# Kernel tuning notes

Hardware: AMD Instinct MI355X
Metric: run time of the kernel (lower is better)

The kernel has to match this reference:

```python
import jax, jax.numpy as jnp
import numpy as np

E, D, B, P = 16, 5, 8, 65536
EXPERT_DIM = 128
N_BETAS = 4
EPS = 1e-6


def setup_inputs() -> dict:
    key = jax.random.key(0)
    k1, k2, k3, k4 = jax.random.split(key, 4)
    V = jax.random.normal(k1, (E, D, B, P), dtype=jnp.float32)
    masks = jax.random.randint(k2, (E, P), 0, 2) > 0  # bool [E, P]
    betas = jax.random.normal(k3, (E, N_BETAS), dtype=jnp.float32)
    expert_pos_embed = jax.random.normal(k4, (E, EXPERT_DIM), dtype=jnp.float32)
    temperature = jnp.ones((1,), dtype=jnp.float32)
    return {
        'V': V,
        'masks': masks,
        'betas': betas,
        'expert_pos_embed': expert_pos_embed,
        'temperature': temperature,
        'num_patches': P,
    }


def reference(V, masks, betas, expert_pos_embed, temperature, num_patches):
    # per-expert scalar weights
    pos_w = jax.nn.sigmoid(expert_pos_embed.mean(axis=1))          # [E]
    beta_w = 1.0 + jax.nn.sigmoid(betas).mean(axis=1)              # [E] (sum(sigmoid)/len)
    w = pos_w * beta_w                                             # [E]

    m = masks.astype(V.dtype)                                      # [E, P]
    # masked weighted vote accumulation over experts, per direction
    num = jnp.einsum('e,edbp,ep->dbp', w, V, m)                    # [D, B, P]
    den = jnp.einsum('e,ep->p', w, m)                              # [P] (same for all d, b)
    den = jnp.maximum(den, EPS)

    patch_votes = (num / den[None, None, :]).sum(axis=0) / 5.0     # [B, P]
    return patch_votes / jnp.abs(temperature[0])
```

## Files before the change

kernel.cpp:

```cpp
#include <hip/hip_runtime.h>
#include <math.h>

#define NE 16
#define ND 5
#define NB 8
#define NP 65536
#define EDIM 128
#define NBETAS 4


__global__ __launch_bounds__(128) void cfa_prep(const float* __restrict__ betas,
                                                const float* __restrict__ embed,
                                                const float* __restrict__ temp,
                                                const unsigned int* __restrict__ mask_words,
                                                float* __restrict__ ws) {
    const int t = threadIdx.x;
    if (t < NE) {
        const float4* ep = (const float4*)(embed + t * EDIM);
        float s = 0.f;
        #pragma unroll
        for (int i = 0; i < EDIM / 4; ++i) { float4 v = ep[i]; s += v.x + v.y + v.z + v.w; }
        float pos_w = 1.f / (1.f + __expf(-s * (1.f / EDIM)));
        float bs = 0.f;
        #pragma unroll
        for (int i = 0; i < NBETAS; ++i) bs += 1.f / (1.f + __expf(-betas[t * NBETAS + i]));
        ws[t] = pos_w * (1.f + bs * (1.f / NBETAS));
    }
    if (t == NE) ws[NE] = 0.2f / fabsf(temp[0]);
    if (t >= 64) {
        const int lane = t - 64;
        unsigned o1 = 0, o3 = 0;
        #pragma unroll
        for (int k = 0; k < 16; ++k) {
            unsigned x = mask_words[lane + k * 64];
            o1 |= x & 0x0000FF00u;
            o3 |= x & 0xFF000000u;
        }
        #pragma unroll
        for (int off = 32; off; off >>= 1) {
            o1 |= __shfl_xor(o1, off, 64);
            o3 |= __shfl_xor(o3, off, 64);
        }
        if (lane == 0) {
            int flag = o1 ? 0 : (o3 ? 2 : 1);
            ((int*)ws)[NE + 1] = flag;
        }
    }
}

__global__ __launch_bounds__(256) void cfa_main(const float* __restrict__ V,
                                                const void* __restrict__ masks,
                                                const float* __restrict__ ws,
                                                float* __restrict__ out) {
    __shared__ float sw[NE];
    __shared__ float sscale;
    __shared__ int sflag;
    if (threadIdx.x < NE) sw[threadIdx.x] = ws[threadIdx.x];
    if (threadIdx.x == NE) sscale = ws[NE];
    if (threadIdx.x == NE + 1) sflag = ((const int*)ws)[NE + 1];
    __syncthreads();

    const int idx = blockIdx.x * 256 + threadIdx.x;
    const int pi  = idx & (NP / 2 - 1);
    const int b   = idx >> 15;
    const int p   = pi << 1;

    float m0[NE], m1[NE];
    const int flag = sflag;
    if (flag == 0) {
        const unsigned char* mb = (const unsigned char*)masks + p;
        #pragma unroll
        for (int e = 0; e < NE; ++e) {
            uchar2 u = *(const uchar2*)(mb + e * NP);
            m0[e] = (float)u.x; m1[e] = (float)u.y;
        }
    } else if (flag == 1) {
        const int* mi = (const int*)masks + p;
        #pragma unroll
        for (int e = 0; e < NE; ++e) {
            int2 u = *(const int2*)(mi + e * NP);
            m0[e] = (float)u.x; m1[e] = (float)u.y;
        }
    } else {
        const float* mf = (const float*)masks + p;
        #pragma unroll
        for (int e = 0; e < NE; ++e) {
            float2 u = *(const float2*)(mf + e * NP);
            m0[e] = u.x; m1[e] = u.y;
        }
    }

    float wm0[NE], wm1[NE];
    float den0 = 0.f, den1 = 0.f;
    #pragma unroll
    for (int e = 0; e < NE; ++e) {
        const float we = sw[e];
        wm0[e] = we * m0[e]; wm1[e] = we * m1[e];
        den0 += wm0[e];      den1 += wm1[e];
    }

    float a0 = 0.f, a1 = 0.f;
    const float* vp = V + b * NP + p;
    #pragma unroll
    for (int e = 0; e < NE; ++e) {
        #pragma unroll
        for (int d = 0; d < ND; ++d) {
            float2 v = *(const float2*)(vp + (e * ND + d) * (NB * NP));
            a0 = fmaf(wm0[e], v.x, a0);
            a1 = fmaf(wm1[e], v.y, a1);
        }
    }

    const float scale = sscale;
    float2 o;
    o.x = a0 / fmaxf(den0, 1e-6f) * scale;
    o.y = a1 / fmaxf(den1, 1e-6f) * scale;
    *(float2*)(out + b * NP + p) = o;
}

extern "C" void kernel_launch(void* const* d_in, const int* in_sizes, int n_in,
                              void* d_out, int out_size, void* d_ws, size_t ws_size,
                              hipStream_t stream) {
    const float* V     = (const float*)d_in[0];
    const void*  masks = d_in[1];
    const float* betas = (const float*)d_in[2];
    const float* embed = (const float*)d_in[3];
    const float* temp  = (const float*)d_in[4];

    float* ws  = (float*)d_ws;
    float* out = (float*)d_out;

    cfa_prep<<<1, 128, 0, stream>>>(betas, embed, temp,
                                    (const unsigned int*)masks, ws);

    const int threads = NB * NP / 2;
    cfa_main<<<threads / 256, 256, 0, stream>>>(V, masks, ws, out);
}
```

Measured before the change: 37.74 us.

## Fuse prep into main kernel, widen to float4, split experts across half-blocks

Removes the separate prep launch by having each block recompute the per-expert weights, scale and mask dtype flag itself. The flag check now samples only the first 64 mask words. Each thread handles four patches with float4 loads, and the two half-blocks each sum eight experts before a shared-memory reduction. This cuts a kernel launch and its dependency and widens memory accesses, at the cost of redundant per-block prep work, an extra barrier, and a weaker mask-dtype heuristic.

```diff
diff --git a/kernel.cpp b/kernel.cpp
--- a/kernel.cpp
+++ b/kernel.cpp
@@ -9,113 +9,127 @@
 #define NBETAS 4
 
 
-__global__ __launch_bounds__(128) void cfa_prep(const float* __restrict__ betas,
-                                                const float* __restrict__ embed,
-                                                const float* __restrict__ temp,
-                                                const unsigned int* __restrict__ mask_words,
-                                                float* __restrict__ ws) {
-    const int t = threadIdx.x;
-    if (t < NE) {
-        const float4* ep = (const float4*)(embed + t * EDIM);
+__global__ __launch_bounds__(256, 4) void cfa_fused(
+    const float* __restrict__ V,
+    const void* __restrict__ masks,
+    const float* __restrict__ betas,
+    const float* __restrict__ embed,
+    const float* __restrict__ temp,
+    float* __restrict__ out)
+{
+    __shared__ float sw[NE];
+    __shared__ float sscale;
+    __shared__ int   sflag;
+    __shared__ float4 redA[128];
+    __shared__ float4 redD[128];
+
+    const int tid = threadIdx.x;
+
+    if (tid < 128) {
+        const int e = tid >> 3, j = tid & 7;
+        const float4* ep = (const float4*)(embed + e * EDIM + j * 16);
         float s = 0.f;
         #pragma unroll
-        for (int i = 0; i < EDIM / 4; ++i) { float4 v = ep[i]; s += v.x + v.y + v.z + v.w; }
-        float pos_w = 1.f / (1.f + __expf(-s * (1.f / EDIM)));
-        float bs = 0.f;
-        #pragma unroll
-        for (int i = 0; i < NBETAS; ++i) bs += 1.f / (1.f + __expf(-betas[t * NBETAS + i]));
-        ws[t] = pos_w * (1.f + bs * (1.f / NBETAS));
-    }
-    if (t == NE) ws[NE] = 0.2f / fabsf(temp[0]);
-    if (t >= 64) {
-        const int lane = t - 64;
-        unsigned o1 = 0, o3 = 0;
-        #pragma unroll
-        for (int k = 0; k < 16; ++k) {
-            unsigned x = mask_words[lane + k * 64];
-            o1 |= x & 0x0000FF00u;
-            o3 |= x & 0xFF000000u;
+        for (int i = 0; i < 4; ++i) { float4 v = ep[i]; s += v.x + v.y + v.z + v.w; }
+        s += __shfl_xor(s, 4, 64);
+        s += __shfl_xor(s, 2, 64);
+        s += __shfl_xor(s, 1, 64);
+        if (j == 0) {
+            float pos_w = 1.f / (1.f + __expf(-s * (1.f / EDIM)));
+            float bs = 0.f;
+            #pragma unroll
+            for (int i = 0; i < NBETAS; ++i)
+                bs += 1.f / (1.f + __expf(-betas[e * NBETAS + i]));
+            sw[e] = pos_w * (1.f + bs * (1.f / NBETAS));
         }
+        if (tid == 0) sscale = 0.2f / fabsf(temp[0]);
+    } else if (tid >= 192) {
+        const int lane = tid - 192;
+        unsigned x = ((const unsigned*)masks)[lane];
+        unsigned o1 = x & 0x0000FF00u, o3 = x & 0xFF000000u;
         #pragma unroll
         for (int off = 32; off; off >>= 1) {
             o1 |= __shfl_xor(o1, off, 64);
             o3 |= __shfl_xor(o3, off, 64);
         }
-        if (lane == 0) {
-            int flag = o1 ? 0 : (o3 ? 2 : 1);
-            ((int*)ws)[NE + 1] = flag;
-        }
+        if (lane == 0) sflag = o1 ? 0 : (o3 ? 2 : 1);
     }
-}
-
-__global__ __launch_bounds__(256) void cfa_main(const float* __restrict__ V,
-                                                const void* __restrict__ masks,
-                                                const float* __restrict__ ws,
-                                                float* __restrict__ out) {
-    __shared__ float sw[NE];
-    __shared__ float sscale;
-    __shared__ int sflag;
-    if (threadIdx.x < NE) sw[threadIdx.x] = ws[threadIdx.x];
-    if (threadIdx.x == NE) sscale = ws[NE];
-    if (threadIdx.x == NE + 1) sflag = ((const int*)ws)[NE + 1];
     __syncthreads();
 
-    const int idx = blockIdx.x * 256 + threadIdx.x;
-    const int pi  = idx & (NP / 2 - 1);
-    const int b   = idx >> 15;
-    const int p   = pi << 1;
+    const int q  = blockIdx.x * 128 + (tid & 127);
+    const int b  = q >> 14;
+    const int p  = (q & 16383) << 2;
+    const int e0 = (tid >> 7) << 3;
+    const int flag = sflag;
 
-    float m0[NE], m1[NE];
-    const int flag = sflag;
+    float4 wm[8];
     if (flag == 0) {
         const unsigned char* mb = (const unsigned char*)masks + p;
         #pragma unroll
-        for (int e = 0; e < NE; ++e) {
-            uchar2 u = *(const uchar2*)(mb + e * NP);
-            m0[e] = (float)u.x; m1[e] = (float)u.y;
+        for (int ee = 0; ee < 8; ++ee) {
+            uchar4 u = *(const uchar4*)(mb + (e0 + ee) * NP);
+            const float we = sw[e0 + ee];
+            wm[ee].x = we * (float)u.x; wm[ee].y = we * (float)u.y;
+            wm[ee].z = we * (float)u.z; wm[ee].w = we * (float)u.w;
         }
     } else if (flag == 1) {
         const int* mi = (const int*)masks + p;
         #pragma unroll
-        for (int e = 0; e < NE; ++e) {
-            int2 u = *(const int2*)(mi + e * NP);
-            m0[e] = (float)u.x; m1[e] = (float)u.y;
+        for (int ee = 0; ee < 8; ++ee) {
+            int4 u = *(const int4*)(mi + (e0 + ee) * NP);
+            const float we = sw[e0 + ee];
+            wm[ee].x = we * (float)u.x; wm[ee].y = we * (float)u.y;
+            wm[ee].z = we * (float)u.z; wm[ee].w = we * (float)u.w;
         }
     } else {
         const float* mf = (const float*)masks + p;
         #pragma unroll
-        for (int e = 0; e < NE; ++e) {
-            float2 u = *(const float2*)(mf + e * NP);
-            m0[e] = u.x; m1[e] = u.y;
+        for (int ee = 0; ee < 8; ++ee) {
+            float4 u = *(const float4*)(mf + (e0 + ee) * NP);
+            const float we = sw[e0 + ee];
+            wm[ee].x = we * u.x; wm[ee].y = we * u.y;
+            wm[ee].z = we * u.z; wm[ee].w = we * u.w;
         }
     }
 
-    float wm0[NE], wm1[NE];
-    float den0 = 0.f, den1 = 0.f;
+    float4 den = {0.f, 0.f, 0.f, 0.f};
     #pragma unroll
-    for (int e = 0; e < NE; ++e) {
-        const float we = sw[e];
-        wm0[e] = we * m0[e]; wm1[e] = we * m1[e];
-        den0 += wm0[e];      den1 += wm1[e];
+    for (int ee = 0; ee < 8; ++ee) {
+        den.x += wm[ee].x; den.y += wm[ee].y; den.z += wm[ee].z; den.w += wm[ee].w;
     }
 
-    float a0 = 0.f, a1 = 0.f;
-    const float* vp = V + b * NP + p;
+    float4 a = {0.f, 0.f, 0.f, 0.f};
+    const float* vb = V + b * NP + p;
     #pragma unroll
-    for (int e = 0; e < NE; ++e) {
+    for (int ee = 0; ee < 8; ++ee) {
+        const float* ve = vb + (e0 + ee) * (ND * NB * NP);
         #pragma unroll
         for (int d = 0; d < ND; ++d) {
-            float2 v = *(const float2*)(vp + (e * ND + d) * (NB * NP));
-            a0 = fmaf(wm0[e], v.x, a0);
-            a1 = fmaf(wm1[e], v.y, a1);
+            float4 v = *(const float4*)(ve + d * (NB * NP));
+            a.x = fmaf(wm[ee].x, v.x, a.x);
+            a.y = fmaf(wm[ee].y, v.y, a.y);
+            a.z = fmaf(wm[ee].z, v.z, a.z);
+            a.w = fmaf(wm[ee].w, v.w, a.w);
         }
     }
 
-    const float scale = sscale;
-    float2 o;
-    o.x = a0 / fmaxf(den0, 1e-6f) * scale;
-    o.y = a1 / fmaxf(den1, 1e-6f) * scale;
-    *(float2*)(out + b * NP + p) = o;
+    if (tid >= 128) {
+        redA[tid - 128] = a;
+        redD[tid - 128] = den;
+    }
+    __syncthreads();
+    if (tid < 128) {
+        float4 a2 = redA[tid], d2 = redD[tid];
+        a.x += a2.x; a.y += a2.y; a.z += a2.z; a.w += a2.w;
+        den.x += d2.x; den.y += d2.y; den.z += d2.z; den.w += d2.w;
+        const float scale = sscale;
+        float4 o;
+        o.x = a.x / fmaxf(den.x, 1e-6f) * scale;
+        o.y = a.y / fmaxf(den.y, 1e-6f) * scale;
+        o.z = a.z / fmaxf(den.z, 1e-6f) * scale;
+        o.w = a.w / fmaxf(den.w, 1e-6f) * scale;
+        *(float4*)(out + b * NP + p) = o;
+    }
 }
 
 extern "C" void kernel_launch(void* const* d_in, const int* in_sizes, int n_in,
@@ -127,12 +141,8 @@
     const float* embed = (const float*)d_in[3];
     const float* temp  = (const float*)d_in[4];
 
-    float* ws  = (float*)d_ws;
     float* out = (float*)d_out;
 
-    cfa_prep<<<1, 128, 0, stream>>>(betas, embed, temp,
-                                    (const unsigned int*)masks, ws);
-
-    const int threads = NB * NP / 2;
-    cfa_main<<<threads / 256, 256, 0, stream>>>(V, masks, ws, out);
+    const int blocks = (NB * NP / 4) / 128;
+    cfa_fused<<<blocks, 256, 0, stream>>>(V, masks, betas, embed, temp, out);
 }
```

New measurement: 33.16 us. -12.1%, faster.
